# Kernel tuning notes

Measured on AMD Instinct MI355X. Metric: run time of the kernel, lower is better.

Reference implementation:

```python
import jax, jax.numpy as jnp
import numpy as np

IN_F = 1024
OUT_F = 1024
GRID_SIZE = 8
GRID_LO, GRID_HI = -2.0, 2.0


def _grid_and_inv_denom():
    grid = jnp.linspace(GRID_LO, GRID_HI, GRID_SIZE)  # [G]
    inv_denom = 1.0 / (float((GRID_HI - GRID_LO) / (GRID_SIZE - 1)) + 1e-06)
    return grid, inv_denom


def setup_inputs() -> dict:
    key = jax.random.key(0)
    kx, kw, ks = jax.random.split(key, 3)
    x = jax.random.normal(kx, (4, 2048, IN_F), dtype=jnp.float32)
    # kaiming_uniform_(a=sqrt(5)) on [out,in]: bound = sqrt(6/((1+a^2)*fan_in)) = sqrt(1/fan_in)
    bound = float(np.sqrt(1.0 / IN_F))
    base_w = jax.random.uniform(kw, (OUT_F, IN_F), minval=-bound, maxval=bound, dtype=jnp.float32)
    base_b = jnp.zeros((OUT_F,), dtype=jnp.float32)
    spline_w = 0.02 * jax.random.normal(ks, (OUT_F, IN_F, GRID_SIZE), dtype=jnp.float32)
    return {"x": x, "base_w": base_w, "base_b": base_b, "spline_w": spline_w}


def reference(x, base_w, base_b, spline_w):
    grid, inv_denom = _grid_and_inv_denom()
    lead = x.shape[:-1]
    x_flat = x.reshape(-1, IN_F)  # [B, in]
    # base path: Linear(SiLU(x))
    base_out = jax.nn.silu(x_flat) @ base_w.T + base_b  # [B, out]
    # RBF basis expansion: [B, in, G]
    basis = jnp.exp(-(((x_flat[..., None] - grid) * inv_denom) ** 2))
    spline_out = jnp.einsum('big,oig->bo', basis, spline_w)  # [B, out]
    out = base_out + spline_out
    return out.reshape(*lead, OUT_F)
```

## Files before the change

kernel.cpp:

```cpp
#include <hip/hip_runtime.h>
#include <stdint.h>

namespace {

constexpr int IN_F = 1024;
constexpr int OUT_F = 1024;
constexpr int GSZ = 8;
constexpr int KTOT = IN_F + IN_F * GSZ;
constexpr int BK = 64;
constexpr int NT = KTOT / BK;
constexpr int NBASE = IN_F / BK;

constexpr int BM = 64, BN = 256;
constexpr int NBLK = OUT_F / BN;
constexpr size_t IMG_BYTES = (size_t)BN * BK * 2;
constexpr size_t WS_NEEDED = (size_t)NBLK * NT * IMG_BYTES;

constexpr double H_D     = 4.0 / 7.0;
constexpr double INVD_D  = 1.0 / (H_D + 1e-6);
constexpr double L2E_D   = 1.4426950408889634;
constexpr double SQL2E_D = 1.2011224087864498;
constexpr double CS_D    = INVD_D * SQL2E_D;
constexpr double DLT_D   = H_D * CS_D;

using short8 = __attribute__((ext_vector_type(8))) short;
using f32x4  = __attribute__((ext_vector_type(4))) float;

__device__ __forceinline__ unsigned cvt_pk(float lo, float hi) {
  unsigned r;
  asm("v_cvt_pk_bf16_f32 %0, %1, %2" : "=v"(r) : "v"(lo), "v"(hi));
  return r;
}
__device__ __forceinline__ float silu_f(float v) {
  float e = __builtin_amdgcn_exp2f(-v * (float)L2E_D);
  return v * __builtin_amdgcn_rcpf(1.0f + e);
}
__device__ __forceinline__ int swz(int row, int kk) {
  return (row * 128 + kk * 2) ^ ((row & 7) << 4);
}

__global__ void wprep(const float* __restrict__ bw, const float* __restrict__ sw,
                      char* __restrict__ wimg)
{
  const int total = NBLK * NT * BN * 8;
  for (int idx = blockIdx.x * blockDim.x + threadIdx.x; idx < total;
       idx += gridDim.x * blockDim.x) {
    const int kk8  = idx & 7;
    const int row  = (idx >> 3) & (BN - 1);
    const int rest = idx >> 11;
    const int step = rest % NT;
    const int nb   = rest / NT;
    const int o    = nb * BN + row;
    const int k    = step * BK + kk8 * 8;
    const float* src = (k < IN_F)
      ? (bw + (size_t)o * IN_F + k)
      : (sw + (size_t)o * (size_t)(IN_F * GSZ) + (k - IN_F));
    const float4 a = ((const float4*)src)[0];
    const float4 b = ((const float4*)src)[1];
    int4 v;
    v.x = (int)cvt_pk(a.x, a.y);
    v.y = (int)cvt_pk(a.z, a.w);
    v.z = (int)cvt_pk(b.x, b.y);
    v.w = (int)cvt_pk(b.z, b.w);
    *(int4*)(wimg + (size_t)rest * IMG_BYTES + swz(row, kk8 * 8)) = v;
  }
}

__global__ __launch_bounds__(512, 4)
void kan_fast(const float* __restrict__ x, const float* __restrict__ bb,
              const char* __restrict__ wimg, float* __restrict__ out)
{
  __shared__ char tA[2][BM * BK * 2];

  const int t    = threadIdx.x;
  const int lane = t & 63;
  const int wid  = t >> 6;
  const int wc   = wid * 32;

  const int d   = blockIdx.x;
  const int r8  = d & 7;
  const int nb  = r8 >> 1;
  const int my  = ((d >> 3) << 1) | (r8 & 1);
  const int bm0 = my * BM;
  const int bn0 = nb * BN;
  const char* img = wimg + (size_t)nb * NT * IMG_BYTES;

  const float CSf  = (float)CS_D;
  const float C0f  = (float)(-2.0 * CS_D);
  const float TDLT = (float)(2.0 * DLT_D);
  float Kc[7];
#pragma unroll
  for (int g = 0; g < 7; ++g) {
    const double cg  = (-2.0 + g * H_D) * CS_D;
    const double cg1 = (-2.0 + (g + 1) * H_D) * CS_D;
    Kc[g] = __builtin_amdgcn_exp2f((float)(-DLT_D * (cg + cg1)));
  }

  f32x4 acc[4][2];
#pragma unroll
  for (int m = 0; m < 4; ++m)
#pragma unroll
    for (int n = 0; n < 2; ++n) acc[m][n] = (f32x4)0.0f;

  const int fr = lane & 15;
  const int kq = (lane >> 4) * 8;

  int boff[4];
#pragma unroll
  for (int n = 0; n < 2; ++n)
#pragma unroll
    for (int kh = 0; kh < 2; ++kh)
      boff[n * 2 + kh] = swz(wc + n * 16 + fr, kh * 32 + kq);
  int aoff[8];
#pragma unroll
  for (int m = 0; m < 4; ++m)
#pragma unroll
    for (int kh = 0; kh < 2; ++kh)
      aoff[m * 2 + kh] = swz(m * 16 + fr, kh * 32 + kq);

  float4 xE[2], xO[2];

  const int prow = t >> 3;
  const int pcol = t & 7;

  auto load_x = [&](int step, float4 (&xr)[2]) {
    const int k0 = step * BK;
    if (k0 < IN_F) {
      const float* p = x + (size_t)(bm0 + prow) * IN_F + k0 + pcol * 8;
      xr[0] = ((const float4*)p)[0];
      xr[1] = ((const float4*)p)[1];
    } else {
      const int i0 = (k0 - IN_F) >> 3;
      xr[0].x = x[(size_t)(bm0 + prow) * IN_F + i0 + pcol];
    }
  };

  auto conv_A = [&](int step, const float4 (&xr)[2], char* dstA) {
    char* dst = dstA + swz(prow, pcol * 8);
    if (step < NBASE) {
      unsigned q0 = cvt_pk(silu_f(xr[0].x), silu_f(xr[0].y));
      unsigned q1 = cvt_pk(silu_f(xr[0].z), silu_f(xr[0].w));
      unsigned q2 = cvt_pk(silu_f(xr[1].x), silu_f(xr[1].y));
      unsigned q3 = cvt_pk(silu_f(xr[1].z), silu_f(xr[1].w));
      *(int4*)dst = make_int4(q0, q1, q2, q3);
    } else {
      const float tb = xr[0].x * CSf;
      const float d0 = tb - C0f;
      float e = __builtin_amdgcn_exp2f(-(d0 * d0));
      const float r = __builtin_amdgcn_exp2f(tb * TDLT);
      unsigned q[4];
#pragma unroll
      for (int g = 0; g < 4; ++g) {
        const float a = e;
        const float b = a * r * Kc[2 * g];
        q[g] = cvt_pk(a, b);
        if (g < 3) e = b * r * Kc[2 * g + 1];
      }
      *(int4*)dst = make_int4(q[0], q[1], q[2], q[3]);
    }
  };

  auto step_body = [&](int s, const char* curA, char* nxtA,
                       const float4 (&xconv)[2], float4 (&xload)[2]) {
    short8 br[4];
    const char* bbase = img + (size_t)s * IMG_BYTES;
#pragma unroll
    for (int j = 0; j < 4; ++j)
      br[j] = *(const short8*)(bbase + boff[j]);
    if (s + 2 < NT) load_x(s + 2, xload);
    if (s + 1 < NT) conv_A(s + 1, xconv, nxtA);
    short8 af[4];
    __builtin_amdgcn_s_setprio(1);
#pragma unroll
    for (int m = 0; m < 4; ++m)
      af[m] = *(const short8*)(curA + aoff[m * 2]);
#pragma unroll
    for (int m = 0; m < 4; ++m)
#pragma unroll
      for (int n = 0; n < 2; ++n)
        acc[m][n] = __builtin_amdgcn_mfma_f32_16x16x32_bf16(af[m], br[n * 2], acc[m][n], 0, 0, 0);
#pragma unroll
    for (int m = 0; m < 4; ++m)
      af[m] = *(const short8*)(curA + aoff[m * 2 + 1]);
#pragma unroll
    for (int m = 0; m < 4; ++m)
#pragma unroll
      for (int n = 0; n < 2; ++n)
        acc[m][n] = __builtin_amdgcn_mfma_f32_16x16x32_bf16(af[m], br[n * 2 + 1], acc[m][n], 0, 0, 0);
    __builtin_amdgcn_s_setprio(0);
    __syncthreads();
  };

  load_x(0, xE);
  load_x(1, xO);
  conv_A(0, xE, tA[0]);
  __syncthreads();

  for (int s = 0; s < NT; s += 2) {
    step_body(s,     tA[0], tA[1], xO, xE);
    step_body(s + 1, tA[1], tA[0], xE, xO);
  }

  const int col = lane & 15;
  const int rr  = (lane >> 4) * 4;
#pragma unroll
  for (int m = 0; m < 4; ++m) {
    const int gr = bm0 + m * 16 + rr;
#pragma unroll
    for (int n = 0; n < 2; ++n) {
      const int gc = bn0 + wc + n * 16 + col;
      const float bias = bb[gc];
#pragma unroll
      for (int j = 0; j < 4; ++j)
        out[(size_t)(gr + j) * OUT_F + gc] = acc[m][n][j] + bias;
    }
  }
}

constexpr int SLDK = 64 + 8;

__device__ __forceinline__ unsigned f2bf(float f) {
  unsigned u = __float_as_uint(f);
  return (u + 0x7fffu + ((u >> 16) & 1u)) >> 16;
}
__device__ __forceinline__ unsigned pk2(float lo, float hi) {
  return f2bf(lo) | (f2bf(hi) << 16);
}

__global__ __launch_bounds__(256)
void kan_slow(const float* __restrict__ x, const float* __restrict__ bw,
              const float* __restrict__ bb, const float* __restrict__ sw,
              float* __restrict__ out)
{
  __shared__ unsigned short tA[128][SLDK];
  __shared__ unsigned short tB[128][SLDK];

  const int t    = threadIdx.x;
  const int lane = t & 63;
  const int wid  = t >> 6;
  const int wr   = (wid >> 1) * 64;
  const int wc   = (wid & 1) * 64;
  const int bm0  = blockIdx.x * 128;
  const int bn0  = blockIdx.y * 128;

  const float CS = (float)CS_D;
  float gsc[GSZ];
#pragma unroll
  for (int g = 0; g < GSZ; ++g)
    gsc[g] = (float)((-2.0 + g * H_D) * CS_D);

  f32x4 acc[4][4];
#pragma unroll
  for (int m = 0; m < 4; ++m)
#pragma unroll
    for (int n = 0; n < 4; ++n) acc[m][n] = (f32x4)0.0f;

  float4 rA[8], rB[8];
  const int rw = t >> 4;
  const int cw = (t & 15) * 4;

  auto load_tile = [&](int step) {
    const int k0 = step * BK;
    const bool base = (k0 < IN_F);
#pragma unroll
    for (int j = 0; j < 8; ++j) {
      const int row = j * 16 + rw;
      const float* p = base
        ? (bw + (size_t)(bn0 + row) * IN_F + k0 + cw)
        : (sw + (size_t)(bn0 + row) * (size_t)(IN_F * GSZ) + (k0 - IN_F) + cw);
      rB[j] = *(const float4*)p;
    }
    if (base) {
#pragma unroll
      for (int j = 0; j < 8; ++j) {
        const int row = j * 16 + rw;
        rA[j] = *(const float4*)(x + (size_t)(bm0 + row) * IN_F + k0 + cw);
      }
    } else {
      const int i0  = (k0 - IN_F) >> 3;
      const int row = t >> 1;
      rA[0] = *(const float4*)(x + (size_t)(bm0 + row) * IN_F + i0 + (t & 1) * 4);
    }
  };

  auto store_tile = [&](int step) {
    const int k0 = step * BK;
    const bool base = (k0 < IN_F);
#pragma unroll
    for (int j = 0; j < 8; ++j) {
      const int row = j * 16 + rw;
      uint2 v;
      v.x = pk2(rB[j].x, rB[j].y);
      v.y = pk2(rB[j].z, rB[j].w);
      *(uint2*)&tB[row][cw] = v;
    }
    if (base) {
#pragma unroll
      for (int j = 0; j < 8; ++j) {
        const int row = j * 16 + rw;
        uint2 v;
        v.x = pk2(silu_f(rA[j].x), silu_f(rA[j].y));
        v.y = pk2(silu_f(rA[j].z), silu_f(rA[j].w));
        *(uint2*)&tA[row][cw] = v;
      }
    } else {
      const int row  = t >> 1;
      const int half = t & 1;
      const float* xv = (const float*)&rA[0];
#pragma unroll
      for (int c = 0; c < 4; ++c) {
        const float tb = xv[c] * CS;
        union { unsigned u[4]; int4 v4; } pkv;
#pragma unroll
        for (int g = 0; g < 8; g += 2) {
          const float t0 = tb - gsc[g];
          const float t1 = tb - gsc[g + 1];
          const float e0 = __builtin_amdgcn_exp2f(-(t0 * t0));
          const float e1 = __builtin_amdgcn_exp2f(-(t1 * t1));
          pkv.u[g >> 1] = pk2(e0, e1);
        }
        const int kc = (half * 4 + c) * 8;
        *(int4*)&tA[row][kc] = pkv.v4;
      }
    }
  };

  auto compute_tile = [&]() {
    const int r  = lane & 15;
    const int kq = (lane >> 4) * 8;
#pragma unroll
    for (int kh = 0; kh < 2; ++kh) {
      short8 af[4], bf[4];
#pragma unroll
      for (int m = 0; m < 4; ++m)
        af[m] = *(const short8*)&tA[wr + m * 16 + r][kh * 32 + kq];
#pragma unroll
      for (int n = 0; n < 4; ++n)
        bf[n] = *(const short8*)&tB[wc + n * 16 + r][kh * 32 + kq];
#pragma unroll
      for (int m = 0; m < 4; ++m)
#pragma unroll
        for (int n = 0; n < 4; ++n)
          acc[m][n] = __builtin_amdgcn_mfma_f32_16x16x32_bf16(af[m], bf[n], acc[m][n], 0, 0, 0);
    }
  };

  load_tile(0);
  for (int step = 0; step < NT; ++step) {
    store_tile(step);
    __syncthreads();
    if (step + 1 < NT) load_tile(step + 1);
    compute_tile();
    __syncthreads();
  }

  const int col = lane & 15;
  const int rr  = (lane >> 4) * 4;
#pragma unroll
  for (int m = 0; m < 4; ++m) {
    const int gr = bm0 + wr + m * 16 + rr;
#pragma unroll
    for (int n = 0; n < 4; ++n) {
      const int gc = bn0 + wc + n * 16 + col;
      const float bias = bb[gc];
#pragma unroll
      for (int j = 0; j < 4; ++j)
        out[(size_t)(gr + j) * OUT_F + gc] = acc[m][n][j] + bias;
    }
  }
}

}

extern "C" void kernel_launch(void* const* d_in, const int* in_sizes, int n_in,
                              void* d_out, int out_size, void* d_ws, size_t ws_size,
                              hipStream_t stream) {
  const float *x, *bw, *bb, *sw;
  if (in_sizes[0] == OUT_F) {
    bb = (const float*)d_in[0];
    bw = (const float*)d_in[1];
    sw = (const float*)d_in[2];
    x  = (const float*)d_in[3];
  } else {
    x  = (const float*)d_in[0];
    bw = (const float*)d_in[1];
    bb = (const float*)d_in[2];
    sw = (const float*)d_in[3];
  }
  float* out = (float*)d_out;
  const int rows = (in_sizes[0] == OUT_F) ? in_sizes[3] / IN_F : in_sizes[0] / IN_F;

  if (ws_size >= WS_NEEDED && d_ws != nullptr && (rows % (2 * BM)) == 0) {
    hipLaunchKernelGGL(wprep, dim3(2048), dim3(256), 0, stream, bw, sw, (char*)d_ws);
    const int nblocks = NBLK * (rows / BM);
    hipLaunchKernelGGL(kan_fast, dim3(nblocks), dim3(512), 0, stream,
                       x, bb, (const char*)d_ws, out);
  } else {
    dim3 grid(rows / 128, OUT_F / 128);
    hipLaunchKernelGGL(kan_slow, grid, dim3(256), 0, stream, x, bw, bb, sw, out);
  }
}
```

Measured before the change: 209.4 us.

## Build A fragments in registers directly from x, drop LDS staging

Changes the block tile from 64x256 to 128x128 with a 2x4 wave layout. Each wave now loads x straight from global memory into registers and computes the SiLU and RBF bf16 fragments there, removing the shared-memory A tile, its double buffering and the per-step __syncthreads. The cost is that the basis work is repeated across the four column waves, and each lane issues strided scalar x loads with no prefetch overlapping the MFMAs. The weight-image layout and block mapping are adjusted to the new BN.

Result: slower. 647.1 us (+209.1%).

```diff
diff --git a/kernel.cpp b/kernel.cpp
--- a/kernel.cpp
+++ b/kernel.cpp
@@ -11,7 +11,7 @@
 constexpr int NT = KTOT / BK;
 constexpr int NBASE = IN_F / BK;
 
-constexpr int BM = 64, BN = 256;
+constexpr int BM = 128, BN = 128;
 constexpr int NBLK = OUT_F / BN;
 constexpr size_t IMG_BYTES = (size_t)BN * BK * 2;
 constexpr size_t WS_NEEDED = (size_t)NBLK * NT * IMG_BYTES;
@@ -34,6 +34,11 @@
 __device__ __forceinline__ float silu_f(float v) {
   float e = __builtin_amdgcn_exp2f(-v * (float)L2E_D);
   return v * __builtin_amdgcn_rcpf(1.0f + e);
+}
+__device__ __forceinline__ short8 pk4_to_s8(unsigned q0, unsigned q1, unsigned q2, unsigned q3) {
+  union { int4 v; short8 s; } u;
+  u.v = make_int4((int)q0, (int)q1, (int)q2, (int)q3);
+  return u.s;
 }
 __device__ __forceinline__ int swz(int row, int kk) {
   return (row * 128 + kk * 2) ^ ((row & 7) << 4);
@@ -47,7 +52,7 @@
        idx += gridDim.x * blockDim.x) {
     const int kk8  = idx & 7;
     const int row  = (idx >> 3) & (BN - 1);
-    const int rest = idx >> 11;
+    const int rest = idx >> 10;
     const int step = rest % NT;
     const int nb   = rest / NT;
     const int o    = nb * BN + row;
@@ -70,17 +75,15 @@
 void kan_fast(const float* __restrict__ x, const float* __restrict__ bb,
               const char* __restrict__ wimg, float* __restrict__ out)
 {
-  __shared__ char tA[2][BM * BK * 2];
-
   const int t    = threadIdx.x;
   const int lane = t & 63;
   const int wid  = t >> 6;
-  const int wc   = wid * 32;
+  const int wr   = (wid >> 2) * 64;
+  const int wc   = (wid & 3) * 32;
 
   const int d   = blockIdx.x;
-  const int r8  = d & 7;
-  const int nb  = r8 >> 1;
-  const int my  = ((d >> 3) << 1) | (r8 & 1);
+  const int nb  = d & 7;
+  const int my  = d >> 3;
   const int bm0 = my * BM;
   const int bn0 = nb * BN;
   const char* img = wimg + (size_t)nb * NT * IMG_BYTES;
@@ -103,7 +106,8 @@
     for (int n = 0; n < 2; ++n) acc[m][n] = (f32x4)0.0f;
 
   const int fr = lane & 15;
-  const int kq = (lane >> 4) * 8;
+  const int cq = lane >> 4;
+  const int kq = cq * 8;
 
   int boff[4];
 #pragma unroll
@@ -111,101 +115,88 @@
 #pragma unroll
     for (int kh = 0; kh < 2; ++kh)
       boff[n * 2 + kh] = swz(wc + n * 16 + fr, kh * 32 + kq);
-  int aoff[8];
+
+  const float* xrow[4];
 #pragma unroll
   for (int m = 0; m < 4; ++m)
-#pragma unroll
-    for (int kh = 0; kh < 2; ++kh)
-      aoff[m * 2 + kh] = swz(m * 16 + fr, kh * 32 + kq);
-
-  float4 xE[2], xO[2];
-
-  const int prow = t >> 3;
-  const int pcol = t & 7;
-
-  auto load_x = [&](int step, float4 (&xr)[2]) {
-    const int k0 = step * BK;
-    if (k0 < IN_F) {
-      const float* p = x + (size_t)(bm0 + prow) * IN_F + k0 + pcol * 8;
-      xr[0] = ((const float4*)p)[0];
-      xr[1] = ((const float4*)p)[1];
-    } else {
-      const int i0 = (k0 - IN_F) >> 3;
-      xr[0].x = x[(size_t)(bm0 + prow) * IN_F + i0 + pcol];
-    }
-  };
-
-  auto conv_A = [&](int step, const float4 (&xr)[2], char* dstA) {
-    char* dst = dstA + swz(prow, pcol * 8);
-    if (step < NBASE) {
-      unsigned q0 = cvt_pk(silu_f(xr[0].x), silu_f(xr[0].y));
-      unsigned q1 = cvt_pk(silu_f(xr[0].z), silu_f(xr[0].w));
-      unsigned q2 = cvt_pk(silu_f(xr[1].x), silu_f(xr[1].y));
-      unsigned q3 = cvt_pk(silu_f(xr[1].z), silu_f(xr[1].w));
-      *(int4*)dst = make_int4(q0, q1, q2, q3);
-    } else {
-      const float tb = xr[0].x * CSf;
-      const float d0 = tb - C0f;
-      float e = __builtin_amdgcn_exp2f(-(d0 * d0));
-      const float r = __builtin_amdgcn_exp2f(tb * TDLT);
-      unsigned q[4];
-#pragma unroll
-      for (int g = 0; g < 4; ++g) {
-        const float a = e;
-        const float b = a * r * Kc[2 * g];
-        q[g] = cvt_pk(a, b);
-        if (g < 3) e = b * r * Kc[2 * g + 1];
-      }
-      *(int4*)dst = make_int4(q[0], q[1], q[2], q[3]);
-    }
-  };
-
-  auto step_body = [&](int s, const char* curA, char* nxtA,
-                       const float4 (&xconv)[2], float4 (&xload)[2]) {
+    xrow[m] = x + (size_t)(bm0 + wr + m * 16 + fr) * IN_F;
+
+  for (int s = 0; s < NT; ++s) {
     short8 br[4];
     const char* bbase = img + (size_t)s * IMG_BYTES;
 #pragma unroll
     for (int j = 0; j < 4; ++j)
       br[j] = *(const short8*)(bbase + boff[j]);
-    if (s + 2 < NT) load_x(s + 2, xload);
-    if (s + 1 < NT) conv_A(s + 1, xconv, nxtA);
-    short8 af[4];
+
+    short8 af[8];
+    if (s < NBASE) {
+      const int k0 = s * BK;
+#pragma unroll
+      for (int kh = 0; kh < 2; ++kh) {
+        float4 v0[4], v1[4];
+#pragma unroll
+        for (int m = 0; m < 4; ++m) {
+          const float* p = xrow[m] + k0 + kh * 32 + kq;
+          v0[m] = ((const float4*)p)[0];
+          v1[m] = ((const float4*)p)[1];
+        }
+#pragma unroll
+        for (int m = 0; m < 4; ++m) {
+          unsigned q0 = cvt_pk(silu_f(v0[m].x), silu_f(v0[m].y));
+          unsigned q1 = cvt_pk(silu_f(v0[m].z), silu_f(v0[m].w));
+          unsigned q2 = cvt_pk(silu_f(v1[m].x), silu_f(v1[m].y));
+          unsigned q3 = cvt_pk(silu_f(v1[m].z), silu_f(v1[m].w));
+          af[m * 2 + kh] = pk4_to_s8(q0, q1, q2, q3);
+        }
+      }
+    } else {
+      const int ib = (s - NBASE) * 8 + cq;
+      float xv[4][2];
+#pragma unroll
+      for (int m = 0; m < 4; ++m) {
+        xv[m][0] = xrow[m][ib];
+        xv[m][1] = xrow[m][ib + 4];
+      }
+#pragma unroll
+      for (int m = 0; m < 4; ++m) {
+#pragma unroll
+        for (int kh = 0; kh < 2; ++kh) {
+          const float tb = xv[m][kh] * CSf;
+          const float d0 = tb - C0f;
+          float e = __builtin_amdgcn_exp2f(-(d0 * d0));
+          const float r = __builtin_amdgcn_exp2f(tb * TDLT);
+          unsigned q[4];
+#pragma unroll
+          for (int g = 0; g < 4; ++g) {
+            const float a = e;
+            const float b = a * r * Kc[2 * g];
+            q[g] = cvt_pk(a, b);
+            if (g < 3) e = b * r * Kc[2 * g + 1];
+          }
+          af[m * 2 + kh] = pk4_to_s8(q[0], q[1], q[2], q[3]);
+        }
+      }
+    }
+
     __builtin_amdgcn_s_setprio(1);
 #pragma unroll
     for (int m = 0; m < 4; ++m)
-      af[m] = *(const short8*)(curA + aoff[m * 2]);
+#pragma unroll
+      for (int n = 0; n < 2; ++n)
+        acc[m][n] = __builtin_amdgcn_mfma_f32_16x16x32_bf16(af[m * 2], br[n * 2], acc[m][n], 0, 0, 0);
 #pragma unroll
     for (int m = 0; m < 4; ++m)
 #pragma unroll
       for (int n = 0; n < 2; ++n)
-        acc[m][n] = __builtin_amdgcn_mfma_f32_16x16x32_bf16(af[m], br[n * 2], acc[m][n], 0, 0, 0);
-#pragma unroll
-    for (int m = 0; m < 4; ++m)
-      af[m] = *(const short8*)(curA + aoff[m * 2 + 1]);
-#pragma unroll
-    for (int m = 0; m < 4; ++m)
-#pragma unroll
-      for (int n = 0; n < 2; ++n)
-        acc[m][n] = __builtin_amdgcn_mfma_f32_16x16x32_bf16(af[m], br[n * 2 + 1], acc[m][n], 0, 0, 0);
+        acc[m][n] = __builtin_amdgcn_mfma_f32_16x16x32_bf16(af[m * 2 + 1], br[n * 2 + 1], acc[m][n], 0, 0, 0);
     __builtin_amdgcn_s_setprio(0);
-    __syncthreads();
-  };
-
-  load_x(0, xE);
-  load_x(1, xO);
-  conv_A(0, xE, tA[0]);
-  __syncthreads();
-
-  for (int s = 0; s < NT; s += 2) {
-    step_body(s,     tA[0], tA[1], xO, xE);
-    step_body(s + 1, tA[1], tA[0], xE, xO);
   }
 
   const int col = lane & 15;
   const int rr  = (lane >> 4) * 4;
 #pragma unroll
   for (int m = 0; m < 4; ++m) {
-    const int gr = bm0 + m * 16 + rr;
+    const int gr = bm0 + wr + m * 16 + rr;
 #pragma unroll
     for (int n = 0; n < 2; ++n) {
       const int gc = bn0 + wc + n * 16 + col;
@@ -390,7 +381,7 @@
   float* out = (float*)d_out;
   const int rows = (in_sizes[0] == OUT_F) ? in_sizes[3] / IN_F : in_sizes[0] / IN_F;
 
-  if (ws_size >= WS_NEEDED && d_ws != nullptr && (rows % (2 * BM)) == 0) {
+  if (ws_size >= WS_NEEDED && d_ws != nullptr && (rows % BM) == 0) {
     hipLaunchKernelGGL(wprep, dim3(2048), dim3(256), 0, stream, bw, sw, (char*)d_ws);
     const int nblocks = NBLK * (rows / BM);
     hipLaunchKernelGGL(kan_fast, dim3(nblocks), dim3(512), 0, stream,
```
